# Optimization experiments

Hardware: AMD Instinct MI355X
Metric: run time of the kernel (lower is better)

## Reference

```python
import jax, jax.numpy as jnp
import numpy as np

N_NODES = 100000
N_EDGES = 1600000
IN_F = 256
OUT_F = 128


def setup_inputs() -> dict:
    key = jax.random.key(0)
    k1, k2, k3, k4, k5, k6 = jax.random.split(key, 6)
    x = jax.random.normal(k1, (N_NODES, IN_F), dtype=jnp.float32)
    edge_row = jax.random.randint(k2, (N_EDGES,), 0, N_NODES)  # destination (output row)
    edge_col = jax.random.randint(k3, (N_EDGES,), 0, N_NODES)  # source (gathered node)
    edge_val = jax.random.uniform(k4, (N_EDGES,), dtype=jnp.float32)  # normalized adj weights
    # Xavier-uniform init like nn.init.xavier_uniform_
    limit = float(np.sqrt(6.0 / (IN_F + OUT_F)))
    weight = jax.random.uniform(k5, (IN_F, OUT_F), dtype=jnp.float32, minval=-limit, maxval=limit)
    bias = jnp.zeros((OUT_F,), dtype=jnp.float32)
    return {"x": x, "edge_row": edge_row, "edge_col": edge_col,
            "edge_val": edge_val, "weight": weight, "bias": bias}


def reference(x, edge_row, edge_col, edge_val, weight, bias):
    # Dense transform: h = x @ W + b   -> [N, OUT_F]
    h = x @ weight + bias
    # Sparse adjacency matmul: out[i] = sum_{e: row[e]==i} val[e] * h[col[e]]
    msg = h[edge_col] * edge_val[:, None]  # [E, OUT_F] gather + scale
    out = jax.ops.segment_sum(msg, edge_row, num_segments=N_NODES)
    return out
```

## Files before the change

kernel.cpp:

```cpp
#include <hip/hip_runtime.h>

#define IN_F 256
#define OUT_F 128
#define CAP 5120
#define EPB 8192

typedef __attribute__((ext_vector_type(8))) short short8;
typedef __attribute__((ext_vector_type(4))) float floatx4;
typedef __attribute__((ext_vector_type(2))) float floatx2;

__device__ __forceinline__ unsigned short f2bf(float f) {
    union { float f; unsigned int u; } v; v.f = f;
    unsigned int u = v.u;
    unsigned int r = (u + 0x7FFFu + ((u >> 16) & 1u)) >> 16;
    return (unsigned short)r;
}

__global__ __launch_bounds__(256) void prep_kernel(
    const float* __restrict__ w, unsigned short* __restrict__ w_t,
    int* __restrict__ cursor, int nb)
{
    const int g = blockIdx.x * 256 + threadIdx.x;
    if (g < IN_F * OUT_F) {
        const int n = g >> 8;
        const int k = g & 255;
        w_t[n * 256 + k] = f2bf(w[k * OUT_F + n]);
    }
    if (g < nb) cursor[g] = 0;
}

#define XS2 264
#define HS2 136
#define GEMM_SMEM 33792

__device__ __forceinline__ void gemm_body(
    char* smem,
    const float* __restrict__ x, const unsigned short* __restrict__ w_t,
    const float* __restrict__ bias, unsigned short* __restrict__ h_bf,
    int tile, int M)
{
    unsigned short* xs = (unsigned short*)smem;

    const int tid  = threadIdx.x;
    const int w    = tid >> 6;
    const int l    = tid & 63;
    const int m16  = l & 15;
    const int g    = l >> 4;
    const int row0 = tile * 64;

    short8 bf[2][8];
    #pragma unroll
    for (int nt = 0; nt < 2; nt++)
        #pragma unroll
        for (int ks = 0; ks < 8; ks++)
            bf[nt][ks] = *(const short8*)(
                w_t + (w * 32 + nt * 16 + m16) * 256 + ks * 32 + g * 8);

    #pragma unroll
    for (int s = 0; s < 16; s++) {
        const int idx = tid + s * 256;
        const int row = idx >> 6;
        const int c4  = idx & 63;
        const int gr  = row0 + row;
        float4 v = make_float4(0.f, 0.f, 0.f, 0.f);
        if (gr < M) v = *(const float4*)(x + (size_t)gr * IN_F + c4 * 4);
        ushort4 b;
        b.x = f2bf(v.x); b.y = f2bf(v.y); b.z = f2bf(v.z); b.w = f2bf(v.w);
        *(ushort4*)(xs + row * XS2 + c4 * 4) = b;
    }
    __syncthreads();

    floatx4 acc[4][2];
    #pragma unroll
    for (int mt = 0; mt < 4; mt++) {
        acc[mt][0] = (floatx4){0.f, 0.f, 0.f, 0.f};
        acc[mt][1] = (floatx4){0.f, 0.f, 0.f, 0.f};
    }

    #pragma unroll
    for (int ks = 0; ks < 8; ks++) {
        #pragma unroll
        for (int mt = 0; mt < 4; mt++) {
            const short8 a = *(const short8*)(xs + (mt * 16 + m16) * XS2 + ks * 32 + g * 8);
            acc[mt][0] = __builtin_amdgcn_mfma_f32_16x16x32_bf16(a, bf[0][ks], acc[mt][0], 0, 0, 0);
            acc[mt][1] = __builtin_amdgcn_mfma_f32_16x16x32_bf16(a, bf[1][ks], acc[mt][1], 0, 0, 0);
        }
    }
    __syncthreads();

    unsigned short* hs = xs;
    #pragma unroll
    for (int nt = 0; nt < 2; nt++) {
        const int col = w * 32 + nt * 16 + m16;
        const float bv = bias[col];
        #pragma unroll
        for (int mt = 0; mt < 4; mt++)
            #pragma unroll
            for (int r = 0; r < 4; r++)
                hs[(mt * 16 + g * 4 + r) * HS2 + col] = f2bf(acc[mt][nt][r] + bv);
    }
    __syncthreads();

    {
        const int row = tid >> 2;
        const int seg = tid & 3;
        const int gr  = row0 + row;
        if (gr < M) {
            #pragma unroll
            for (int q = 0; q < 4; q++) {
                const uint4 v = *(const uint4*)(hs + row * HS2 + seg * 32 + q * 8);
                *(uint4*)(h_bf + (size_t)gr * OUT_F + seg * 32 + q * 8) = v;
            }
        }
    }
}

__device__ __forceinline__ void sort_body(
    char* smem, const int* __restrict__ erow, const int* __restrict__ ecol,
    const float* __restrict__ eval, int* __restrict__ cursor,
    uint2* __restrict__ tmp, int E, int nb, int blk)
{
    int* lcnt  = (int*)smem;
    int* lbase = lcnt + 512;
    for (int i = threadIdx.x; i < nb; i += 256) lcnt[i] = 0;
    __syncthreads();
    const int base = blk * EPB;

    unsigned int rec[EPB / 256];
    #pragma unroll
    for (int i = 0; i < EPB / 256; i++) {
        const int e = base + i * 256 + threadIdx.x;
        rec[i] = 0xFFFFFFFFu;
        if (e < E) {
            const int r = erow[e];
            const int b = r >> 8;
            const int lp = atomicAdd(&lcnt[b], 1);
            rec[i] = ((unsigned int)lp << 17) | ((unsigned int)(r & 255) << 9)
                   | (unsigned int)b;
        }
    }
    __syncthreads();

    for (int i = threadIdx.x; i < nb; i += 256) {
        const int c = lcnt[i];
        lbase[i] = c ? atomicAdd(&cursor[i], c) : 0;
    }
    __syncthreads();

    #pragma unroll
    for (int i = 0; i < EPB / 256; i++) {
        if (rec[i] != 0xFFFFFFFFu) {
            const int e  = base + i * 256 + threadIdx.x;
            const int b  = rec[i] & 511;
            const int rl = (rec[i] >> 9) & 255;
            const int lp = rec[i] >> 17;
            const int pos = lbase[b] + lp;
            if (pos < CAP)
                tmp[(size_t)b * CAP + pos] = make_uint2(
                    ((unsigned int)rl << 24) | (unsigned int)ecol[e],
                    __float_as_uint(eval[e]));
        }
    }
}

__global__ __launch_bounds__(256) void k_sort_gemm(
    const int* __restrict__ erow, const int* __restrict__ ecol,
    const float* __restrict__ eval, int* __restrict__ cursor,
    uint2* __restrict__ tmp, int E, int nb, int EB,
    const float* __restrict__ x, const unsigned short* __restrict__ w_t,
    const float* __restrict__ bias, unsigned short* __restrict__ h_bf, int M)
{
    __shared__ __align__(16) char smem[GEMM_SMEM];
    if ((int)blockIdx.x < EB)
        sort_body(smem, erow, ecol, eval, cursor, tmp, E, nb, blockIdx.x);
    else
        gemm_body(smem, x, w_t, bias, h_bf, (int)blockIdx.x - EB, M);
}

__global__ __launch_bounds__(1024, 8) void k_csrgather(
    const uint2* __restrict__ tmp, const int* __restrict__ cursor,
    const unsigned short* __restrict__ h_bf, float* __restrict__ out, int M)
{
    __shared__ int nh[256], nst[256], ncur[256];
    __shared__ unsigned int lcv[CAP];

    const int b  = blockIdx.x;
    const size_t tb = (size_t)b * CAP;
    const int cnt = min(cursor[b], CAP);
    const int t  = threadIdx.x;

    if (t < 256) nh[t] = 0;
    __syncthreads();
    for (int i = t; i < cnt; i += 1024) atomicAdd(&nh[tmp[tb + i].x >> 24], 1);
    __syncthreads();

    int v = 0;
    if (t < 256) { v = nh[t]; nst[t] = v; }
    __syncthreads();
    for (int off = 1; off < 256; off <<= 1) {
        int u = 0;
        if (t < 256 && t >= off) u = nst[t - off];
        __syncthreads();
        if (t < 256) nst[t] += u;
        __syncthreads();
    }
    if (t < 256) {
        const int ex = nst[t] - v;
        nst[t]  = ex;
        ncur[t] = ex;
    }
    __syncthreads();

    for (int i = t; i < cnt; i += 1024) {
        const uint2 p = tmp[tb + i];
        const int d  = p.x >> 24;
        const int lp = atomicAdd(&ncur[d], 1);
        const float f = __uint_as_float(p.y);
        const int q = min((int)(f * 32768.0f), 32767);
        lcv[lp] = ((p.x & 0x00FFFFFFu) << 15) | (unsigned int)q;
    }
    __syncthreads();

    const int wv   = t >> 6;
    const int lane = t & 63;
    const unsigned int* hp = (const unsigned int*)h_bf;

    for (int k = 0; k < 16; k++) {
        const int nl   = wv + k * 16;
        const int node = b * 256 + nl;
        if (node >= M) continue;
        const int s = nst[nl];
        const int e = ncur[nl];
        float acc0 = 0.f, acc1 = 0.f;
        int j = s;
        for (; j + 8 <= e; j += 8) {
            unsigned int mu[8];
            #pragma unroll
            for (int u = 0; u < 8; u++)
                mu[u] = __builtin_amdgcn_readfirstlane(lcv[j + u]);
            unsigned int p[8];
            #pragma unroll
            for (int u = 0; u < 8; u++)
                p[u] = hp[(size_t)(mu[u] >> 15) * 64 + lane];
            #pragma unroll
            for (int u = 0; u < 8; u++) {
                const float vv = (float)(mu[u] & 0x7FFFu) * (1.0f / 32768.0f) + (0.5f / 32768.0f);
                acc0 += vv * __uint_as_float(p[u] << 16);
                acc1 += vv * __uint_as_float(p[u] & 0xFFFF0000u);
            }
        }
        for (; j < e; j++) {
            const unsigned int mu = __builtin_amdgcn_readfirstlane(lcv[j]);
            const unsigned int p = hp[(size_t)(mu >> 15) * 64 + lane];
            const float vv = (float)(mu & 0x7FFFu) * (1.0f / 32768.0f) + (0.5f / 32768.0f);
            acc0 += vv * __uint_as_float(p << 16);
            acc1 += vv * __uint_as_float(p & 0xFFFF0000u);
        }
        floatx2 o; o.x = acc0; o.y = acc1;
        *(floatx2*)(out + (size_t)node * OUT_F + lane * 2) = o;
    }
}

extern "C" void kernel_launch(void* const* d_in, const int* in_sizes, int n_in,
                              void* d_out, int out_size, void* d_ws, size_t ws_size,
                              hipStream_t stream) {
    const float* x     = (const float*)d_in[0];
    const int*   erow  = (const int*)d_in[1];
    const int*   ecol  = (const int*)d_in[2];
    const float* eval  = (const float*)d_in[3];
    const float* wgt   = (const float*)d_in[4];
    const float* bias  = (const float*)d_in[5];
    float*       out   = (float*)d_out;

    const int M  = in_sizes[0] / IN_F;
    const int E  = in_sizes[1];
    const int nb = (M + 255) >> 8;
    const int EB = (E + EPB - 1) / EPB;
    const int GT = (M + 63) / 64;

    char* ws = (char*)d_ws;
    unsigned short* h_bf = (unsigned short*)ws;  ws += (size_t)M * OUT_F * 2;
    unsigned short* w_t  = (unsigned short*)ws;  ws += (size_t)IN_F * OUT_F * 2;
    int* cursor      = (int*)ws;                 ws += ((size_t)nb * 4 + 15) & ~15ull;
    uint2* tmp       = (uint2*)ws;               ws += (size_t)nb * CAP * 8;

    prep_kernel<<<(IN_F * OUT_F + 255) / 256, 256, 0, stream>>>(wgt, w_t, cursor, nb);

    k_sort_gemm<<<EB + GT, 256, 0, stream>>>(erow, ecol, eval, cursor, tmp, E, nb, EB,
                                             x, w_t, bias, h_bf, M);

    k_csrgather<<<nb, 1024, 0, stream>>>(tmp, cursor, h_bf, out, M);
}
```

Measured before the change: 283.7 us.

## Stage sorted edges in LDS for coalesced bucket writes and single-pass CSR build

The sort phase now does a block-local counting sort in shared memory: it scans the per-bucket counts, stages the records contiguously in LDS, then writes them to the global bucket buffer in runs, replacing scattered 8-byte stores. Edge weights are quantized once in the sort phase rather than in the gather kernel. The gather kernel keeps each edge's local position and payload in registers from the first read of tmp, so tmp is read once instead of twice and the ncur atomics go away. In exchange the edges per block are halved (more blocks and more global cursor atomics), shared memory grows, and a 512-entry scan with many barriers is added.

```diff
diff --git a/kernel.cpp b/kernel.cpp
--- a/kernel.cpp
+++ b/kernel.cpp
@@ -3,7 +3,7 @@
 #define IN_F 256
 #define OUT_F 128
 #define CAP 5120
-#define EPB 8192
+#define EPB 4096
 
 typedef __attribute__((ext_vector_type(8))) short short8;
 typedef __attribute__((ext_vector_type(4))) float floatx4;
@@ -31,7 +31,7 @@
 
 #define XS2 264
 #define HS2 136
-#define GEMM_SMEM 33792
+#define KSMEM 38912
 
 __device__ __forceinline__ void gemm_body(
     char* smem,
@@ -120,16 +120,21 @@
     const float* __restrict__ eval, int* __restrict__ cursor,
     uint2* __restrict__ tmp, int E, int nb, int blk)
 {
-    int* lcnt  = (int*)smem;
-    int* lbase = lcnt + 512;
-    for (int i = threadIdx.x; i < nb; i += 256) lcnt[i] = 0;
+    uint2* stage = (uint2*)smem;
+    int* lcnt  = (int*)(smem + 32768);
+    int* lscan = lcnt + 512;
+    int* lbase = lscan + 512;
+    const int t = threadIdx.x;
+
+    lcnt[t] = 0; lcnt[t + 256] = 0;
     __syncthreads();
     const int base = blk * EPB;
+    const int tot  = min(EPB, E - base);
 
     unsigned int rec[EPB / 256];
     #pragma unroll
     for (int i = 0; i < EPB / 256; i++) {
-        const int e = base + i * 256 + threadIdx.x;
+        const int e = base + i * 256 + t;
         rec[i] = 0xFFFFFFFFu;
         if (e < E) {
             const int r = erow[e];
@@ -141,25 +146,47 @@
     }
     __syncthreads();
 
-    for (int i = threadIdx.x; i < nb; i += 256) {
-        const int c = lcnt[i];
-        lbase[i] = c ? atomicAdd(&cursor[i], c) : 0;
+    lscan[t] = lcnt[t]; lscan[t + 256] = lcnt[t + 256];
+    __syncthreads();
+    for (int off = 1; off < 512; off <<= 1) {
+        const int u0 = (t >= off) ? lscan[t - off] : 0;
+        const int u1 = (t + 256 >= off) ? lscan[t + 256 - off] : 0;
+        __syncthreads();
+        lscan[t] += u0; lscan[t + 256] += u1;
+        __syncthreads();
+    }
+    lscan[t]       -= lcnt[t];
+    lscan[t + 256] -= lcnt[t + 256];
+    {
+        const int c0 = lcnt[t];
+        lbase[t] = c0 ? atomicAdd(&cursor[t], c0) : 0;
+        const int c1 = lcnt[t + 256];
+        lbase[t + 256] = (c1 && t + 256 < nb) ? atomicAdd(&cursor[t + 256], c1) : 0;
     }
     __syncthreads();
 
     #pragma unroll
     for (int i = 0; i < EPB / 256; i++) {
         if (rec[i] != 0xFFFFFFFFu) {
-            const int e  = base + i * 256 + threadIdx.x;
-            const int b  = rec[i] & 511;
-            const int rl = (rec[i] >> 9) & 255;
-            const int lp = rec[i] >> 17;
-            const int pos = lbase[b] + lp;
-            if (pos < CAP)
-                tmp[(size_t)b * CAP + pos] = make_uint2(
-                    ((unsigned int)rl << 24) | (unsigned int)ecol[e],
-                    __float_as_uint(eval[e]));
-        }
+            const int e  = base + i * 256 + t;
+            const unsigned int b  = rec[i] & 511u;
+            const unsigned int rl = (rec[i] >> 9) & 255u;
+            const unsigned int lp = rec[i] >> 17;
+            const float f = eval[e];
+            const int q = min((int)(f * 32768.0f), 32767);
+            stage[lscan[b] + lp] = make_uint2(
+                (rl << 24) | (unsigned int)ecol[e],
+                (b << 15) | (unsigned int)q);
+        }
+    }
+    __syncthreads();
+
+    for (int i = t; i < tot; i += 256) {
+        const uint2 p = stage[i];
+        const unsigned int b = (p.y >> 15) & 0x1FFu;
+        const int pos = lbase[b] + (i - lscan[b]);
+        if (pos < CAP)
+            tmp[(size_t)b * CAP + pos] = p;
     }
 }
 
@@ -170,7 +197,7 @@
     const float* __restrict__ x, const unsigned short* __restrict__ w_t,
     const float* __restrict__ bias, unsigned short* __restrict__ h_bf, int M)
 {
-    __shared__ __align__(16) char smem[GEMM_SMEM];
+    __shared__ __align__(16) char smem[KSMEM];
     if ((int)blockIdx.x < EB)
         sort_body(smem, erow, ecol, eval, cursor, tmp, E, nb, blockIdx.x);
     else
@@ -181,7 +208,7 @@
     const uint2* __restrict__ tmp, const int* __restrict__ cursor,
     const unsigned short* __restrict__ h_bf, float* __restrict__ out, int M)
 {
-    __shared__ int nh[256], nst[256], ncur[256];
+    __shared__ int nh[256], nst[256];
     __shared__ unsigned int lcv[CAP];
 
     const int b  = blockIdx.x;
@@ -191,7 +218,20 @@
 
     if (t < 256) nh[t] = 0;
     __syncthreads();
-    for (int i = t; i < cnt; i += 1024) atomicAdd(&nh[tmp[tb + i].x >> 24], 1);
+
+    unsigned int rec[CAP / 1024]; unsigned int pay[CAP / 1024];
+    #pragma unroll
+    for (int u = 0; u < CAP / 1024; u++) {
+        const int i = u * 1024 + t;
+        rec[u] = 0xFFFFFFFFu;
+        if (i < cnt) {
+            const uint2 p = tmp[tb + i];
+            const int d = p.x >> 24;
+            const int lp = atomicAdd(&nh[d], 1);
+            rec[u] = ((unsigned int)lp << 8) | (unsigned int)d;
+            pay[u] = ((p.x & 0x00FFFFFFu) << 15) | (p.y & 0x7FFFu);
+        }
+    }
     __syncthreads();
 
     int v = 0;
@@ -204,20 +244,13 @@
         if (t < 256) nst[t] += u;
         __syncthreads();
     }
-    if (t < 256) {
-        const int ex = nst[t] - v;
-        nst[t]  = ex;
-        ncur[t] = ex;
-    }
-    __syncthreads();
-
-    for (int i = t; i < cnt; i += 1024) {
-        const uint2 p = tmp[tb + i];
-        const int d  = p.x >> 24;
-        const int lp = atomicAdd(&ncur[d], 1);
-        const float f = __uint_as_float(p.y);
-        const int q = min((int)(f * 32768.0f), 32767);
-        lcv[lp] = ((p.x & 0x00FFFFFFu) << 15) | (unsigned int)q;
+    if (t < 256) nst[t] -= v;
+    __syncthreads();
+
+    #pragma unroll
+    for (int u = 0; u < CAP / 1024; u++) {
+        if (rec[u] != 0xFFFFFFFFu)
+            lcv[nst[rec[u] & 255u] + (rec[u] >> 8)] = pay[u];
     }
     __syncthreads();
 
@@ -230,7 +263,7 @@
         const int node = b * 256 + nl;
         if (node >= M) continue;
         const int s = nst[nl];
-        const int e = ncur[nl];
+        const int e = s + nh[nl];
         float acc0 = 0.f, acc1 = 0.f;
         int j = s;
         for (; j + 8 <= e; j += 8) {
```

New measurement: 274.5 us. -3.2%, faster.
